# Kernel tuning notes

Hardware: AMD Instinct MI355X
Metric: run time of the kernel (lower is better)

The kernel has to match this reference:

```python
import jax, jax.numpy as jnp
import numpy as np

N_NODES = 50000
N_EDGES = 800000


def spmm(edge_src, edge_dst, edge_weight, h):
    # out[i] = sum over edges (src->dst=i) of w * h[src]  == adj @ h
    msgs = h[edge_src] * edge_weight[:, None]  # [E, D]
    return jax.ops.segment_sum(msgs, edge_dst, num_segments=N_NODES)


def setup_inputs() -> dict:
    key = jax.random.key(0)
    ks = jax.random.split(key, 12)
    x = jax.random.normal(ks[0], (N_NODES, 512), dtype=jnp.float32)
    edge_src = jax.random.randint(ks[1], (N_EDGES,), 0, N_NODES, dtype=jnp.int32)
    edge_dst = jax.random.randint(ks[2], (N_EDGES,), 0, N_NODES, dtype=jnp.int32)
    edge_weight = jax.random.uniform(ks[3], (N_EDGES,), dtype=jnp.float32)
    def init_w(k, fin, fout):
        s = 1.0 / np.sqrt(fout)
        return jax.random.uniform(k, (fin, fout), minval=-s, maxval=s, dtype=jnp.float32)
    W1 = init_w(ks[4], 512, 512); b1 = jnp.zeros((512,), jnp.float32)
    W2 = init_w(ks[5], 512, 256); b2 = jnp.zeros((256,), jnp.float32)
    W3 = init_w(ks[6], 256, 128); b3 = jnp.zeros((128,), jnp.float32)
    W4 = init_w(ks[7], 128, 64);  b4 = jnp.zeros((64,), jnp.float32)
    return {"x": x, "edge_src": edge_src, "edge_dst": edge_dst,
            "edge_weight": edge_weight, "W1": W1, "b1": b1, "W2": W2,
            "b2": b2, "W3": W3, "b3": b3, "W4": W4, "b4": b4}


def reference(x, edge_src, edge_dst, edge_weight, W1, b1, W2, b2, W3, b3, W4, b4):
    # GraphConvolution: out = adj @ (x @ W) + b ; dropout is identity in eval mode
    def gc(h, W, b):
        return spmm(edge_src, edge_dst, edge_weight, h @ W) + b
    h = jax.nn.relu(gc(x, W1, b1))
    h = jax.nn.relu(gc(h, W2, b2))
    h = jax.nn.relu(gc(h, W3, b3))
    emb = gc(h, W4, b4)
    return emb
```

## Files before the change

### kernel.cpp

```cpp
#include <hip/hip_runtime.h>

#define NN 50000
#define NE 800000
#define SCAN_BLOCKS 196

typedef __attribute__((ext_vector_type(8))) short short8;
typedef __attribute__((ext_vector_type(4))) float float4v;

struct us4 { unsigned short x, y, z, w; };
struct us8 { unsigned short v[8]; };

__device__ __forceinline__ unsigned short f2bf(float f) {
    unsigned u = __float_as_uint(f);
    unsigned r = (u + 0x7FFF + ((u >> 16) & 1)) >> 16;
    return (unsigned short)r;
}

__device__ __forceinline__ float bf2f(unsigned short u) {
    return __uint_as_float((unsigned)u << 16);
}

__device__ __forceinline__ void gload_lds16(const unsigned short* g, unsigned short* l) {
    __builtin_amdgcn_global_load_lds(
        (const __attribute__((address_space(1))) unsigned int*)g,
        (__attribute__((address_space(3))) unsigned int*)l,
        16, 0, 0);
}

template <int BM, int BN, int WM, int WN, int OUTBF>
__global__ __launch_bounds__(256) void gemm_mfma(const unsigned short* __restrict__ A,
                                                 const unsigned short* __restrict__ Bt,
                                                 void* __restrict__ Cv,
                                                 int N, int K, int M) {
    constexpr int BK = 32;
    constexpr int MT = WM / 16;
    constexpr int NT = WN / 16;
    constexpr int WCOLS = BN / WN;

    __shared__ __align__(16) unsigned short As[BM * BK];
    __shared__ __align__(16) unsigned short Bs[BN * BK];

    const int tid = threadIdx.x;
    const int lane = tid & 63;
    const int wid = tid >> 6;
    const int col16 = lane & 15;
    const int q = lane >> 4;
    const int wr = (wid / WCOLS) * WM;
    const int wc = (wid % WCOLS) * WN;
    const int rowBase = blockIdx.y * BM;
    const int colBase = blockIdx.x * BN;

    const int srow = lane >> 2;
    const int scol = (lane & 3) * 8;

    float4v acc[MT][NT];
#pragma unroll
    for (int t = 0; t < MT; ++t)
#pragma unroll
        for (int u = 0; u < NT; ++u)
            acc[t][u] = (float4v)0.f;

    for (int k0 = 0; k0 < K; k0 += BK) {
        __syncthreads();
#pragma unroll
        for (int l = wid; l < BM / 16; l += 4) {
            int row = rowBase + 16 * l + srow;
            row = row < N ? row : N - 1;
            gload_lds16(A + (size_t)row * K + k0 + scol, &As[l * 512]);
        }
#pragma unroll
        for (int l = wid; l < BN / 16; l += 4) {
            const int row = colBase + 16 * l + srow;
            gload_lds16(Bt + (size_t)row * K + k0 + scol, &Bs[l * 512]);
        }
        __syncthreads();

        short8 a[MT], b[NT];
#pragma unroll
        for (int t = 0; t < MT; ++t)
            a[t] = *(const short8*)&As[(wr + t * 16 + col16) * BK + q * 8];
#pragma unroll
        for (int u = 0; u < NT; ++u)
            b[u] = *(const short8*)&Bs[(wc + u * 16 + col16) * BK + q * 8];
#pragma unroll
        for (int t = 0; t < MT; ++t)
#pragma unroll
            for (int u = 0; u < NT; ++u)
                acc[t][u] = __builtin_amdgcn_mfma_f32_16x16x32_bf16(a[t], b[u], acc[t][u], 0, 0, 0);
    }

#pragma unroll
    for (int t = 0; t < MT; ++t) {
        const int row0 = rowBase + wr + t * 16 + q * 4;
#pragma unroll
        for (int u = 0; u < NT; ++u) {
            const int col = colBase + wc + u * 16 + col16;
#pragma unroll
            for (int r = 0; r < 4; ++r) {
                const int row = row0 + r;
                if (row < N) {
                    if (OUTBF)
                        ((unsigned short*)Cv)[(size_t)row * M + col] = f2bf(acc[t][u][r]);
                    else
                        ((float*)Cv)[(size_t)row * M + col] = acc[t][u][r];
                }
            }
        }
    }
}

__global__ void cvt_f32_bf16(const float* __restrict__ in, unsigned short* __restrict__ out,
                             long long n4) {
    long long i = (long long)blockIdx.x * blockDim.x + threadIdx.x;
    const long long stride = (long long)gridDim.x * blockDim.x;
    for (; i < n4; i += stride) {
        const float4 v = *(const float4*)&in[i * 4];
        us4 o = {f2bf(v.x), f2bf(v.y), f2bf(v.z), f2bf(v.w)};
        *(us4*)&out[i * 4] = o;
    }
}

__global__ void cvt_transpose_all(const float* __restrict__ W1, unsigned short* __restrict__ Wt1,
                                  const float* __restrict__ W2, unsigned short* __restrict__ Wt2,
                                  const float* __restrict__ W3, unsigned short* __restrict__ Wt3,
                                  const float* __restrict__ W4, unsigned short* __restrict__ Wt4) {
    int idx = blockIdx.x * blockDim.x + threadIdx.x;
    const float* W; unsigned short* Wt; int K, M;
    if (idx < 262144)      { W = W1; Wt = Wt1; K = 512; M = 512; }
    else if (idx < 393216) { idx -= 262144; W = W2; Wt = Wt2; K = 512; M = 256; }
    else if (idx < 425984) { idx -= 393216; W = W3; Wt = Wt3; K = 256; M = 128; }
    else if (idx < 434176) { idx -= 425984; W = W4; Wt = Wt4; K = 128; M = 64; }
    else return;
    const int k = idx / M;
    const int m = idx % M;
    Wt[(size_t)m * K + k] = f2bf(W[(size_t)k * M + m]);
}

__global__ void zero_counts(int* __restrict__ counts) {
    int i = blockIdx.x * blockDim.x + threadIdx.x;
    if (i < NN) counts[i] = 0;
}

__global__ void hist_dst(const int* __restrict__ dst, int* __restrict__ counts) {
    int i = blockIdx.x * blockDim.x + threadIdx.x;
    const int stride = gridDim.x * blockDim.x;
    for (; i < NE; i += stride) atomicAdd(&counts[dst[i]], 1);
}

__global__ __launch_bounds__(256) void scan_partial(const int* __restrict__ counts,
                                                    int* __restrict__ partials) {
    __shared__ int r[256];
    const int t = threadIdx.x;
    const int i = blockIdx.x * 256 + t;
    r[t] = (i < NN) ? counts[i] : 0;
    __syncthreads();
    for (int s = 128; s > 0; s >>= 1) {
        if (t < s) r[t] += r[t + s];
        __syncthreads();
    }
    if (t == 0) partials[blockIdx.x] = r[0];
}

__global__ __launch_bounds__(256) void scan_base(const int* __restrict__ partials,
                                                 int* __restrict__ bases,
                                                 int* __restrict__ offs) {
    __shared__ int s[256];
    const int t = threadIdx.x;
    const int v = (t < SCAN_BLOCKS) ? partials[t] : 0;
    s[t] = v;
    __syncthreads();
    for (int off = 1; off < 256; off <<= 1) {
        int x = (t >= off) ? s[t - off] : 0;
        __syncthreads();
        s[t] += x;
        __syncthreads();
    }
    if (t < SCAN_BLOCKS) bases[t] = s[t] - v;
    if (t == 255) offs[NN] = s[255];
}

__global__ __launch_bounds__(256) void scan_final(int* __restrict__ counts,
                                                  const int* __restrict__ bases,
                                                  int* __restrict__ offs) {
    __shared__ int s[256];
    const int t = threadIdx.x;
    const int i = blockIdx.x * 256 + t;
    const int v = (i < NN) ? counts[i] : 0;
    s[t] = v;
    __syncthreads();
    for (int off = 1; off < 256; off <<= 1) {
        int x = (t >= off) ? s[t - off] : 0;
        __syncthreads();
        s[t] += x;
        __syncthreads();
    }
    if (i < NN) {
        const int e = bases[blockIdx.x] + s[t] - v;
        offs[i] = e;
        counts[i] = e;
    }
}

__global__ void fill_csr(const int* __restrict__ src, const int* __restrict__ dst,
                         const float* __restrict__ w, int* __restrict__ cursor,
                         int* __restrict__ csr_src, float* __restrict__ csr_w) {
    int i = blockIdx.x * blockDim.x + threadIdx.x;
    const int stride = gridDim.x * blockDim.x;
    for (; i < NE; i += stride) {
        const int p = atomicAdd(&cursor[dst[i]], 1);
        csr_src[p] = src[i];
        csr_w[p] = w[i];
    }
}

template <int D, int RELU, int OUTBF>
__global__ __launch_bounds__(256) void spmm_gather(const int* __restrict__ offs,
                                                   const int* __restrict__ csr_src,
                                                   const float* __restrict__ csr_w,
                                                   const unsigned short* __restrict__ hp,
                                                   const float* __restrict__ bias,
                                                   void* __restrict__ outv,
                                                   int dbase, int dstride) {
    constexpr int TPN = D / 8;
    constexpr int NPB = 256 / TPN;
    const int tid = threadIdx.x;
    const int node = blockIdx.x * NPB + tid / TPN;
    const int d = dbase + (tid % TPN) * 8;
    if (node >= NN) return;
    const int beg = offs[node];
    const int end = offs[node + 1];

    float acc[8] = {};
    int j = beg;
    for (; j + 4 <= end; j += 4) {
        const int s0 = csr_src[j];
        const int s1 = csr_src[j + 1];
        const int s2 = csr_src[j + 2];
        const int s3 = csr_src[j + 3];
        const float w0 = csr_w[j];
        const float w1 = csr_w[j + 1];
        const float w2 = csr_w[j + 2];
        const float w3 = csr_w[j + 3];
        const us8 h0 = *(const us8*)&hp[(long long)s0 * dstride + d];
        const us8 h1 = *(const us8*)&hp[(long long)s1 * dstride + d];
        const us8 h2 = *(const us8*)&hp[(long long)s2 * dstride + d];
        const us8 h3 = *(const us8*)&hp[(long long)s3 * dstride + d];
#pragma unroll
        for (int k = 0; k < 8; ++k)
            acc[k] += w0 * bf2f(h0.v[k]) + w1 * bf2f(h1.v[k])
                    + w2 * bf2f(h2.v[k]) + w3 * bf2f(h3.v[k]);
    }
    for (; j < end; ++j) {
        const int s0 = csr_src[j];
        const float w0 = csr_w[j];
        const us8 h0 = *(const us8*)&hp[(long long)s0 * dstride + d];
#pragma unroll
        for (int k = 0; k < 8; ++k)
            acc[k] += w0 * bf2f(h0.v[k]);
    }
#pragma unroll
    for (int k = 0; k < 8; ++k) {
        acc[k] += bias[d + k];
        if (RELU) acc[k] = fmaxf(acc[k], 0.f);
    }
    if (OUTBF) {
        us8 o;
#pragma unroll
        for (int k = 0; k < 8; ++k) o.v[k] = f2bf(acc[k]);
        *(us8*)((unsigned short*)outv + (long long)node * dstride + d) = o;
    } else {
        float* op = (float*)outv + (long long)node * dstride + d;
        *(float4*)op = make_float4(acc[0], acc[1], acc[2], acc[3]);
        *(float4*)(op + 4) = make_float4(acc[4], acc[5], acc[6], acc[7]);
    }
}

extern "C" void kernel_launch(void* const* d_in, const int* in_sizes, int n_in,
                              void* d_out, int out_size, void* d_ws, size_t ws_size,
                              hipStream_t stream) {
    const float* x    = (const float*)d_in[0];
    const int*   esrc = (const int*)d_in[1];
    const int*   edst = (const int*)d_in[2];
    const float* ew   = (const float*)d_in[3];
    const float* W1 = (const float*)d_in[4];  const float* b1 = (const float*)d_in[5];
    const float* W2 = (const float*)d_in[6];  const float* b2 = (const float*)d_in[7];
    const float* W3 = (const float*)d_in[8];  const float* b3 = (const float*)d_in[9];
    const float* W4 = (const float*)d_in[10]; const float* b4 = (const float*)d_in[11];
    float* out = (float*)d_out;

    char* ws = (char*)d_ws;
    int*   offs    = (int*)ws;                    ws += (NN + 1) * sizeof(int);
    int*   counts  = (int*)ws;                    ws += NN * sizeof(int);
    int*   partials= (int*)ws;                    ws += 256 * sizeof(int);
    int*   bases   = (int*)ws;                    ws += 256 * sizeof(int);
    int*   csr_src = (int*)ws;                    ws += NE * sizeof(int);
    float* csr_w   = (float*)ws;                  ws += NE * sizeof(float);
    unsigned short* Wt1 = (unsigned short*)ws;    ws += 512 * 512 * sizeof(unsigned short);
    unsigned short* Wt2 = (unsigned short*)ws;    ws += 256 * 512 * sizeof(unsigned short);
    unsigned short* Wt3 = (unsigned short*)ws;    ws += 128 * 256 * sizeof(unsigned short);
    unsigned short* Wt4 = (unsigned short*)ws;    ws += 64 * 128 * sizeof(unsigned short);
    ws = (char*)(((uintptr_t)ws + 255) & ~(uintptr_t)255);
    unsigned short* tmp = (unsigned short*)ws;    ws += (size_t)NN * 512 * sizeof(unsigned short);
    ws = (char*)(((uintptr_t)ws + 255) & ~(uintptr_t)255);
    unsigned short* hb = (unsigned short*)ws;

    zero_counts<<<(NN + 255) / 256, 256, 0, stream>>>(counts);
    hist_dst<<<3125, 256, 0, stream>>>(edst, counts);
    scan_partial<<<SCAN_BLOCKS, 256, 0, stream>>>(counts, partials);
    scan_base<<<1, 256, 0, stream>>>(partials, bases, offs);
    scan_final<<<SCAN_BLOCKS, 256, 0, stream>>>(counts, bases, offs);
    fill_csr<<<3125, 256, 0, stream>>>(esrc, edst, ew, counts, csr_src, csr_w);

    cvt_f32_bf16<<<12800, 256, 0, stream>>>(x, hb, (long long)NN * 512 / 4);
    cvt_transpose_all<<<(434176 + 255) / 256, 256, 0, stream>>>(W1, Wt1, W2, Wt2, W3, Wt3, W4, Wt4);

    const int nby128 = (NN + 127) / 128;
    const int nby64  = (NN + 63) / 64;

    gemm_mfma<128, 128, 64, 64, 1><<<dim3(4, nby128), 256, 0, stream>>>(hb, Wt1, tmp, NN, 512, 512);
    spmm_gather<256, 1, 1><<<NN / 8, 256, 0, stream>>>(offs, csr_src, csr_w, tmp, b1, hb, 0, 512);
    spmm_gather<256, 1, 1><<<NN / 8, 256, 0, stream>>>(offs, csr_src, csr_w, tmp, b1, hb, 256, 512);
    gemm_mfma<128, 128, 64, 64, 1><<<dim3(2, nby128), 256, 0, stream>>>(hb, Wt2, tmp, NN, 512, 256);
    spmm_gather<256, 1, 1><<<NN / 8, 256, 0, stream>>>(offs, csr_src, csr_w, tmp, b2, hb, 0, 256);
    gemm_mfma<64, 128, 32, 64, 1><<<dim3(1, nby64), 256, 0, stream>>>(hb, Wt3, tmp, NN, 256, 128);
    spmm_gather<128, 1, 1><<<NN / 16, 256, 0, stream>>>(offs, csr_src, csr_w, tmp, b3, hb, 0, 128);
    gemm_mfma<64, 64, 32, 32, 1><<<dim3(1, nby64), 256, 0, stream>>>(hb, Wt4, tmp, NN, 128, 64);
    spmm_gather<64, 0, 0><<<(NN + 31) / 32, 256, 0, stream>>>(offs, csr_src, csr_w, tmp, b4, out, 0, 64);
}
```

Baseline: 607.8 us.

## Double-buffer GEMM LDS, pack CSR as int2, fuse convert with histogram, deepen gather unroll

The GEMM now double-buffers its LDS tiles, issuing the next K-slice's global-to-LDS loads before computing the current one, and needs one barrier per iteration instead of two. The grid is also swapped so consecutive blocks walk rows. CSR source and weight are packed into a single int2 array so the gather makes one 8-byte load per edge, and the gather loop is unrolled to 8 edges to keep more loads in flight. The x conversion and the dst histogram are merged into one launch to cut a kernel launch and let the two overlap. Double buffering doubles LDS use per block and can lower occupancy.

```diff
diff --git a/kernel.cpp b/kernel.cpp
--- a/kernel.cpp
+++ b/kernel.cpp
@@ -3,12 +3,14 @@
 #define NN 50000
 #define NE 800000
 #define SCAN_BLOCKS 196
+#define CVT_BLOCKS 12800
+#define HIST_BLOCKS 3125
 
 typedef __attribute__((ext_vector_type(8))) short short8;
 typedef __attribute__((ext_vector_type(4))) float float4v;
 
-struct us4 { unsigned short x, y, z, w; };
-struct us8 { unsigned short v[8]; };
+struct __align__(8) us4 { unsigned short x, y, z, w; };
+struct __align__(16) us8 { unsigned short v[8]; };
 
 __device__ __forceinline__ unsigned short f2bf(float f) {
     unsigned u = __float_as_uint(f);
@@ -37,8 +39,8 @@
     constexpr int NT = WN / 16;
     constexpr int WCOLS = BN / WN;
 
-    __shared__ __align__(16) unsigned short As[BM * BK];
-    __shared__ __align__(16) unsigned short Bs[BN * BK];
+    __shared__ __align__(16) unsigned short As[2][BM * BK];
+    __shared__ __align__(16) unsigned short Bs[2][BN * BK];
 
     const int tid = threadIdx.x;
     const int lane = tid & 63;
@@ -47,8 +49,8 @@
     const int q = lane >> 4;
     const int wr = (wid / WCOLS) * WM;
     const int wc = (wid % WCOLS) * WN;
-    const int rowBase = blockIdx.y * BM;
-    const int colBase = blockIdx.x * BN;
+    const int rowBase = blockIdx.x * BM;
+    const int colBase = blockIdx.y * BN;
 
     const int srow = lane >> 2;
     const int scol = (lane & 3) * 8;
@@ -60,34 +62,45 @@
         for (int u = 0; u < NT; ++u)
             acc[t][u] = (float4v)0.f;
 
-    for (int k0 = 0; k0 < K; k0 += BK) {
-        __syncthreads();
+    auto stage = [&](int buf, int k0) {
 #pragma unroll
         for (int l = wid; l < BM / 16; l += 4) {
             int row = rowBase + 16 * l + srow;
             row = row < N ? row : N - 1;
-            gload_lds16(A + (size_t)row * K + k0 + scol, &As[l * 512]);
+            gload_lds16(A + (size_t)row * K + k0 + scol, &As[buf][l * 512]);
         }
 #pragma unroll
         for (int l = wid; l < BN / 16; l += 4) {
             const int row = colBase + 16 * l + srow;
-            gload_lds16(Bt + (size_t)row * K + k0 + scol, &Bs[l * 512]);
-        }
-        __syncthreads();
-
+            gload_lds16(Bt + (size_t)row * K + k0 + scol, &Bs[buf][l * 512]);
+        }
+    };
+
+    auto compute = [&](int buf) {
         short8 a[MT], b[NT];
 #pragma unroll
         for (int t = 0; t < MT; ++t)
-            a[t] = *(const short8*)&As[(wr + t * 16 + col16) * BK + q * 8];
+            a[t] = *(const short8*)&As[buf][(wr + t * 16 + col16) * BK + q * 8];
 #pragma unroll
         for (int u = 0; u < NT; ++u)
-            b[u] = *(const short8*)&Bs[(wc + u * 16 + col16) * BK + q * 8];
+            b[u] = *(const short8*)&Bs[buf][(wc + u * 16 + col16) * BK + q * 8];
 #pragma unroll
         for (int t = 0; t < MT; ++t)
 #pragma unroll
             for (int u = 0; u < NT; ++u)
                 acc[t][u] = __builtin_amdgcn_mfma_f32_16x16x32_bf16(a[t], b[u], acc[t][u], 0, 0, 0);
-    }
+    };
+
+    stage(0, 0);
+    __syncthreads();
+    int cur = 0;
+    for (int k0 = BK; k0 < K; k0 += BK) {
+        stage(cur ^ 1, k0);
+        compute(cur);
+        __syncthreads();
+        cur ^= 1;
+    }
+    compute(cur);
 
 #pragma unroll
     for (int t = 0; t < MT; ++t) {
@@ -109,14 +122,22 @@
     }
 }
 
-__global__ void cvt_f32_bf16(const float* __restrict__ in, unsigned short* __restrict__ out,
-                             long long n4) {
-    long long i = (long long)blockIdx.x * blockDim.x + threadIdx.x;
-    const long long stride = (long long)gridDim.x * blockDim.x;
-    for (; i < n4; i += stride) {
-        const float4 v = *(const float4*)&in[i * 4];
-        us4 o = {f2bf(v.x), f2bf(v.y), f2bf(v.z), f2bf(v.w)};
-        *(us4*)&out[i * 4] = o;
+__global__ void cvt_hist(const float* __restrict__ in, unsigned short* __restrict__ out,
+                         const int* __restrict__ dst, int* __restrict__ counts) {
+    const int b = blockIdx.x;
+    if (b < CVT_BLOCKS) {
+        const long long n4 = (long long)NN * 512 / 4;
+        long long i = (long long)b * 256 + threadIdx.x;
+        const long long stride = (long long)CVT_BLOCKS * 256;
+        for (; i < n4; i += stride) {
+            const float4 v = *(const float4*)&in[i * 4];
+            us4 o = {f2bf(v.x), f2bf(v.y), f2bf(v.z), f2bf(v.w)};
+            *(us4*)&out[i * 4] = o;
+        }
+    } else {
+        int i = (b - CVT_BLOCKS) * 256 + threadIdx.x;
+        const int stride = HIST_BLOCKS * 256;
+        for (; i < NE; i += stride) atomicAdd(&counts[dst[i]], 1);
     }
 }
 
@@ -141,12 +162,6 @@
     if (i < NN) counts[i] = 0;
 }
 
-__global__ void hist_dst(const int* __restrict__ dst, int* __restrict__ counts) {
-    int i = blockIdx.x * blockDim.x + threadIdx.x;
-    const int stride = gridDim.x * blockDim.x;
-    for (; i < NE; i += stride) atomicAdd(&counts[dst[i]], 1);
-}
-
 __global__ __launch_bounds__(256) void scan_partial(const int* __restrict__ counts,
                                                     int* __restrict__ partials) {
     __shared__ int r[256];
@@ -203,20 +218,18 @@
 
 __global__ void fill_csr(const int* __restrict__ src, const int* __restrict__ dst,
                          const float* __restrict__ w, int* __restrict__ cursor,
-                         int* __restrict__ csr_src, float* __restrict__ csr_w) {
+                         int2* __restrict__ csr) {
     int i = blockIdx.x * blockDim.x + threadIdx.x;
     const int stride = gridDim.x * blockDim.x;
     for (; i < NE; i += stride) {
         const int p = atomicAdd(&cursor[dst[i]], 1);
-        csr_src[p] = src[i];
-        csr_w[p] = w[i];
+        csr[p] = make_int2(src[i], __float_as_int(w[i]));
     }
 }
 
 template <int D, int RELU, int OUTBF>
 __global__ __launch_bounds__(256) void spmm_gather(const int* __restrict__ offs,
-                                                   const int* __restrict__ csr_src,
-                                                   const float* __restrict__ csr_w,
+                                                   const int2* __restrict__ csr,
                                                    const unsigned short* __restrict__ hp,
                                                    const float* __restrict__ bias,
                                                    void* __restrict__ outv,
@@ -232,31 +245,38 @@
 
     float acc[8] = {};
     int j = beg;
-    for (; j + 4 <= end; j += 4) {
-        const int s0 = csr_src[j];
-        const int s1 = csr_src[j + 1];
-        const int s2 = csr_src[j + 2];
-        const int s3 = csr_src[j + 3];
-        const float w0 = csr_w[j];
-        const float w1 = csr_w[j + 1];
-        const float w2 = csr_w[j + 2];
-        const float w3 = csr_w[j + 3];
-        const us8 h0 = *(const us8*)&hp[(long long)s0 * dstride + d];
-        const us8 h1 = *(const us8*)&hp[(long long)s1 * dstride + d];
-        const us8 h2 = *(const us8*)&hp[(long long)s2 * dstride + d];
-        const us8 h3 = *(const us8*)&hp[(long long)s3 * dstride + d];
+    for (; j + 8 <= end; j += 8) {
+        int2 e[8];
+#pragma unroll
+        for (int t = 0; t < 8; ++t) e[t] = csr[j + t];
+        us8 h[8];
+#pragma unroll
+        for (int t = 0; t < 8; ++t)
+            h[t] = *(const us8*)&hp[(long long)e[t].x * dstride + d];
+#pragma unroll
+        for (int t = 0; t < 8; ++t) {
+            const float w = __int_as_float(e[t].y);
+#pragma unroll
+            for (int k = 0; k < 8; ++k) acc[k] += w * bf2f(h[t].v[k]);
+        }
+    }
+    for (; j + 2 <= end; j += 2) {
+        const int2 e0 = csr[j];
+        const int2 e1 = csr[j + 1];
+        const us8 h0 = *(const us8*)&hp[(long long)e0.x * dstride + d];
+        const us8 h1 = *(const us8*)&hp[(long long)e1.x * dstride + d];
+        const float w0 = __int_as_float(e0.y);
+        const float w1 = __int_as_float(e1.y);
 #pragma unroll
         for (int k = 0; k < 8; ++k)
-            acc[k] += w0 * bf2f(h0.v[k]) + w1 * bf2f(h1.v[k])
-                    + w2 * bf2f(h2.v[k]) + w3 * bf2f(h3.v[k]);
-    }
-    for (; j < end; ++j) {
-        const int s0 = csr_src[j];
-        const float w0 = csr_w[j];
-        const us8 h0 = *(const us8*)&hp[(long long)s0 * dstride + d];
-#pragma unroll
-        for (int k = 0; k < 8; ++k)
-            acc[k] += w0 * bf2f(h0.v[k]);
+            acc[k] += w0 * bf2f(h0.v[k]) + w1 * bf2f(h1.v[k]);
+    }
+    if (j < end) {
+        const int2 e0 = csr[j];
+        const us8 h0 = *(const us8*)&hp[(long long)e0.x * dstride + d];
+        const float w0 = __int_as_float(e0.y);
+#pragma unroll
+        for (int k = 0; k < 8; ++k) acc[k] += w0 * bf2f(h0.v[k]);
     }
 #pragma unroll
     for (int k = 0; k < 8; ++k) {
@@ -293,8 +313,8 @@
     int*   counts  = (int*)ws;                    ws += NN * sizeof(int);
     int*   partials= (int*)ws;                    ws += 256 * sizeof(int);
     int*   bases   = (int*)ws;                    ws += 256 * sizeof(int);
-    int*   csr_src = (int*)ws;                    ws += NE * sizeof(int);
-    float* csr_w   = (float*)ws;                  ws += NE * sizeof(float);
+    ws = (char*)(((uintptr_t)ws + 15) & ~(uintptr_t)15);
+    int2*  csr     = (int2*)ws;                   ws += (size_t)NE * sizeof(int2);
     unsigned short* Wt1 = (unsigned short*)ws;    ws += 512 * 512 * sizeof(unsigned short);
     unsigned short* Wt2 = (unsigned short*)ws;    ws += 256 * 512 * sizeof(unsigned short);
     unsigned short* Wt3 = (unsigned short*)ws;    ws += 128 * 256 * sizeof(unsigned short);
@@ -305,25 +325,23 @@
     unsigned short* hb = (unsigned short*)ws;
 
     zero_counts<<<(NN + 255) / 256, 256, 0, stream>>>(counts);
-    hist_dst<<<3125, 256, 0, stream>>>(edst, counts);
+    cvt_hist<<<CVT_BLOCKS + HIST_BLOCKS, 256, 0, stream>>>(x, hb, edst, counts);
     scan_partial<<<SCAN_BLOCKS, 256, 0, stream>>>(counts, partials);
     scan_base<<<1, 256, 0, stream>>>(partials, bases, offs);
     scan_final<<<SCAN_BLOCKS, 256, 0, stream>>>(counts, bases, offs);
-    fill_csr<<<3125, 256, 0, stream>>>(esrc, edst, ew, counts, csr_src, csr_w);
-
-    cvt_f32_bf16<<<12800, 256, 0, stream>>>(x, hb, (long long)NN * 512 / 4);
+    fill_csr<<<3125, 256, 0, stream>>>(esrc, edst, ew, counts, csr);
     cvt_transpose_all<<<(434176 + 255) / 256, 256, 0, stream>>>(W1, Wt1, W2, Wt2, W3, Wt3, W4, Wt4);
 
     const int nby128 = (NN + 127) / 128;
     const int nby64  = (NN + 63) / 64;
 
-    gemm_mfma<128, 128, 64, 64, 1><<<dim3(4, nby128), 256, 0, stream>>>(hb, Wt1, tmp, NN, 512, 512);
-    spmm_gather<256, 1, 1><<<NN / 8, 256, 0, stream>>>(offs, csr_src, csr_w, tmp, b1, hb, 0, 512);
-    spmm_gather<256, 1, 1><<<NN / 8, 256, 0, stream>>>(offs, csr_src, csr_w, tmp, b1, hb, 256, 512);
-    gemm_mfma<128, 128, 64, 64, 1><<<dim3(2, nby128), 256, 0, stream>>>(hb, Wt2, tmp, NN, 512, 256);
-    spmm_gather<256, 1, 1><<<NN / 8, 256, 0, stream>>>(offs, csr_src, csr_w, tmp, b2, hb, 0, 256);
-    gemm_mfma<64, 128, 32, 64, 1><<<dim3(1, nby64), 256, 0, stream>>>(hb, Wt3, tmp, NN, 256, 128);
-    spmm_gather<128, 1, 1><<<NN / 16, 256, 0, stream>>>(offs, csr_src, csr_w, tmp, b3, hb, 0, 128);
-    gemm_mfma<64, 64, 32, 32, 1><<<dim3(1, nby64), 256, 0, stream>>>(hb, Wt4, tmp, NN, 128, 64);
-    spmm_gather<64, 0, 0><<<(NN + 31) / 32, 256, 0, stream>>>(offs, csr_src, csr_w, tmp, b4, out, 0, 64);
-}
+    gemm_mfma<128, 128, 64, 64, 1><<<dim3(nby128, 4), 256, 0, stream>>>(hb, Wt1, tmp, NN, 512, 512);
+    spmm_gather<256, 1, 1><<<NN / 8, 256, 0, stream>>>(offs, csr, tmp, b1, hb, 0, 512);
+    spmm_gather<256, 1, 1><<<NN / 8, 256, 0, stream>>>(offs, csr, tmp, b1, hb, 256, 512);
+    gemm_mfma<128, 128, 64, 64, 1><<<dim3(nby128, 2), 256, 0, stream>>>(hb, Wt2, tmp, NN, 512, 256);
+    spmm_gather<256, 1, 1><<<NN / 8, 256, 0, stream>>>(offs, csr, tmp, b2, hb, 0, 256);
+    gemm_mfma<64, 128, 32, 64, 1><<<dim3(nby64, 1), 256, 0, stream>>>(hb, Wt3, tmp, NN, 256, 128);
+    spmm_gather<128, 1, 1><<<NN / 16, 256, 0, stream>>>(offs, csr, tmp, b3, hb, 0, 128);
+    gemm_mfma<64, 64, 32, 32, 1><<<dim3(nby64, 1), 256, 0, stream>>>(hb, Wt4, tmp, NN, 128, 64);
+    spmm_gather<64, 0, 0><<<(NN + 31) / 32, 256, 0, stream>>>(offs, csr, tmp, b4, out, 0, 64);
+}
```

Measured after the change: 613.9 us. About the same (+1.0%).
